# Performance work log

Hardware: AMD Instinct MI355X
Metric: run time of the kernel (lower is better)

The kernel has to match this reference:

```python
import jax, jax.numpy as jnp
import numpy as np

B, T, F = 64, 1000, 512
H, KD = 8, 32
EPS = 1e-6


def setup_inputs() -> dict:
    key = jax.random.key(0)
    ks = jax.random.split(key, 12)
    s_in = 1.0 / np.sqrt(F)
    s_out = 1.0 / np.sqrt(H * KD)
    return {
        "x": jax.random.normal(ks[0], (B, T, F), jnp.float32),
        "q": jax.random.normal(ks[1], (F,), jnp.float32) * s_in,      # global_query (1,1,F) squeezed
        "Wq": jax.random.normal(ks[2], (F, H, KD), jnp.float32) * s_in,
        "bq": jnp.zeros((H, KD), jnp.float32),
        "Wk": jax.random.normal(ks[3], (F, H, KD), jnp.float32) * s_in,
        "bk": jnp.zeros((H, KD), jnp.float32),
        "Wv": jax.random.normal(ks[4], (F, H, KD), jnp.float32) * s_in,
        "bv": jnp.zeros((H, KD), jnp.float32),
        "Wo": jax.random.normal(ks[5], (H, KD, F), jnp.float32) * s_out,
        "bo": jnp.zeros((F,), jnp.float32),
        "Wd": jax.random.normal(ks[6], (F, F), jnp.float32) * s_in,    # Dense, use_bias=False
        "gamma": jnp.ones((F,), jnp.float32),
        "beta": jnp.zeros((F,), jnp.float32),
    }


def reference(x, q, Wq, bq, Wk, bk, Wv, bv, Wo, bo, Wd, gamma, beta):
    # Single learned query attends over full sequence (keras MultiHeadAttention semantics).
    qh = jnp.einsum('f,fhk->hk', q, Wq) + bq                   # (H, KD), shared across batch
    kh = jnp.einsum('btf,fhk->bthk', x, Wk) + bk               # (B, T, H, KD)
    vh = jnp.einsum('btf,fhk->bthk', x, Wv) + bv               # (B, T, H, KD)
    scale = 1.0 / jnp.sqrt(jnp.asarray(KD, x.dtype))
    scores = jnp.einsum('hk,bthk->bht', qh, kh) * scale        # (B, H, T)
    attn = jax.nn.softmax(scores, axis=-1)
    ctx = jnp.einsum('bht,bthk->bhk', attn, vh)                # (B, H, KD)
    pooled = jnp.einsum('bhk,hkf->bf', ctx, Wo) + bo           # (B, F) attention output proj
    out = pooled @ Wd                                          # Dense, no bias
    mu = jnp.mean(out, axis=-1, keepdims=True)
    var = jnp.mean(jnp.square(out - mu), axis=-1, keepdims=True)
    return (out - mu) * jax.lax.rsqrt(var + EPS) * gamma + beta
```

## Files before the change

kernel.cpp:

```cpp
#include <hip/hip_runtime.h>
#include <cstddef>

#define B_ 64
#define T_ 1000
#define F_ 512
#define H_ 8
#define KD_ 32
#define HK_ 256
#define NC_ 32

__global__ __launch_bounds__(64) void k_qh(const float* __restrict__ q,
                                           const float* __restrict__ Wq,
                                           const float* __restrict__ bq,
                                           float* __restrict__ qh) {
    int hk = blockIdx.x;
    int lane = threadIdx.x;
    float s = 0.f;
    for (int f = lane; f < F_; f += 64) s += q[f] * Wq[(size_t)f * HK_ + hk];
    #pragma unroll
    for (int off = 32; off; off >>= 1) s += __shfl_down(s, off);
    if (lane == 0) qh[hk] = s + bq[hk];
}

__global__ __launch_bounds__(256) void k_wk(const float* __restrict__ qh,
                                            const float* __restrict__ Wk,
                                            const float* __restrict__ bk,
                                            float* __restrict__ wk,
                                            float* __restrict__ ck) {
    int f = blockIdx.x;
    int tid = threadIdx.x;
    __shared__ float red[256];
    red[tid] = qh[tid] * Wk[(size_t)f * HK_ + tid];
    __syncthreads();
    #pragma unroll
    for (int off = 16; off; off >>= 1) {
        if ((tid & 31) < off) red[tid] += red[tid + off];
        __syncthreads();
    }
    if ((tid & 31) == 0) wk[f * H_ + (tid >> 5)] = red[tid];
    if (f == 0 && tid < H_) {
        float c = 0.f;
        for (int k = 0; k < KD_; k++) c += qh[tid * KD_ + k] * bk[tid * KD_ + k];
        ck[tid] = c;
    }
}

__global__ __launch_bounds__(512) void k_weff(const float* __restrict__ Wo,
                                              const float* __restrict__ Wd,
                                              const float* __restrict__ bo,
                                              float* __restrict__ weff,
                                              float* __restrict__ bwd) {
    int blk = blockIdx.x;
    int f = threadIdx.x;
    if (blk < HK_) {
        const float* wo = Wo + (size_t)blk * F_;
        float s = 0.f;
        for (int g = 0; g < F_; g++) s += wo[g] * Wd[(size_t)g * F_ + f];
        weff[(size_t)blk * F_ + f] = s;
    } else {
        float s = 0.f;
        for (int g = 0; g < F_; g++) s += bo[g] * Wd[(size_t)g * F_ + f];
        bwd[f] = s;
    }
}

__global__ __launch_bounds__(256) void k_fused(const float* __restrict__ x,
                                               const float* __restrict__ wk,
                                               const float* __restrict__ ck,
                                               float* __restrict__ part,
                                               float* __restrict__ ml) {
    int c = blockIdx.x & (NC_ - 1);
    int b = blockIdx.x >> 5;
    int nt = (c < 8) ? 32 : 31;
    int t0 = (c < 8) ? c * 32 : 256 + (c - 8) * 31;
    int tid = threadIdx.x;
    int lane = tid & 63, w = tid >> 6;

    __shared__ float sp[H_][33];

    {
        int f0 = lane * 8;
        float wreg[8][8];
        #pragma unroll
        for (int i = 0; i < 8; i++)
            #pragma unroll
            for (int h = 0; h < H_; h++) wreg[i][h] = wk[(f0 + i) * H_ + h];
        float ckv = ck[lane >> 3];
        const float scale = 0.17677669529663687f;

        for (int tl = w; tl < nt; tl += 4) {
            const float4* xr = (const float4*)(x + ((size_t)(b * T_ + t0 + tl)) * F_ + f0);
            float4 a = xr[0], bb = xr[1];
            float xv[8] = {a.x, a.y, a.z, a.w, bb.x, bb.y, bb.z, bb.w};
            float acc[8];
            #pragma unroll
            for (int h = 0; h < H_; h++) acc[h] = 0.f;
            #pragma unroll
            for (int i = 0; i < 8; i++)
                #pragma unroll
                for (int h = 0; h < H_; h++) acc[h] += xv[i] * wreg[i][h];
            #pragma unroll
            for (int h = 0; h < H_; h++) {
                acc[h] += __shfl_xor(acc[h], 8);
                acc[h] += __shfl_xor(acc[h], 16);
                acc[h] += __shfl_xor(acc[h], 32);
            }
            float v = acc[0];
            #pragma unroll
            for (int h = 1; h < H_; h++) v = ((lane >> 3) == h) ? acc[h] : v;
            v += __shfl_xor(v, 1);
            v += __shfl_xor(v, 2);
            v += __shfl_xor(v, 4);
            if ((lane & 7) == 0) sp[lane >> 3][tl] = (v + ckv) * scale;
        }
    }
    __syncthreads();

    {
        int g = tid >> 5, j = tid & 31;
        float m = -1e30f;
        if (j < nt) m = sp[g][j];
        #pragma unroll
        for (int off = 16; off; off >>= 1) m = fmaxf(m, __shfl_xor(m, off));
        float e0 = 0.f;
        if (j < nt) e0 = __expf(sp[g][j] - m);
        float l = e0;
        __syncthreads();
        if (j < nt) sp[g][j] = e0;
        #pragma unroll
        for (int off = 16; off; off >>= 1) l += __shfl_xor(l, off);
        if (j == 0) {
            float* d = ml + ((size_t)(c * B_ + b) * H_ + g) * 2;
            d[0] = m; d[1] = l;
        }
    }
    __syncthreads();

    {
        float acc[H_][2];
        #pragma unroll
        for (int h = 0; h < H_; h++) { acc[h][0] = 0.f; acc[h][1] = 0.f; }
        const float2* xb = (const float2*)(x + ((size_t)(b * T_ + t0)) * F_) + tid;
        for (int tt = 0; tt < nt; tt++) {
            float2 xv = xb[(size_t)tt * 256];
            #pragma unroll
            for (int h = 0; h < H_; h++) {
                float a = sp[h][tt];
                acc[h][0] += a * xv.x;
                acc[h][1] += a * xv.y;
            }
        }
        float2* dst = (float2*)(part + (size_t)(c * B_ + b) * (H_ * F_));
        #pragma unroll
        for (int h = 0; h < H_; h++)
            dst[h * (F_ / 2) + tid] = make_float2(acc[h][0], acc[h][1]);
    }
}

__global__ __launch_bounds__(256) void k_ctx(const float* __restrict__ part,
                                             const float* __restrict__ Wv,
                                             float* __restrict__ pctx) {
    int b = blockIdx.x & (B_ - 1);
    int p = blockIdx.x >> 6;
    int hk = threadIdx.x;
    int h = hk >> 5;
    const float* p0 = part + ((size_t)((4 * p + 0) * B_ + b) * H_ + h) * F_;
    const float* p1 = part + ((size_t)((4 * p + 1) * B_ + b) * H_ + h) * F_;
    const float* p2 = part + ((size_t)((4 * p + 2) * B_ + b) * H_ + h) * F_;
    const float* p3 = part + ((size_t)((4 * p + 3) * B_ + b) * H_ + h) * F_;
    float a0 = 0.f, a1 = 0.f, a2 = 0.f, a3 = 0.f;
    for (int f = 0; f < F_; f++) {
        float wv = Wv[(size_t)f * HK_ + hk];
        a0 += p0[f] * wv;
        a1 += p1[f] * wv;
        a2 += p2[f] * wv;
        a3 += p3[f] * wv;
    }
    pctx[((size_t)(4 * p + 0) * B_ + b) * HK_ + hk] = a0;
    pctx[((size_t)(4 * p + 1) * B_ + b) * HK_ + hk] = a1;
    pctx[((size_t)(4 * p + 2) * B_ + b) * HK_ + hk] = a2;
    pctx[((size_t)(4 * p + 3) * B_ + b) * HK_ + hk] = a3;
}

__global__ __launch_bounds__(512) void k_tail(const float* __restrict__ pctx,
                                              const float* __restrict__ ml,
                                              const float* __restrict__ bv,
                                              const float* __restrict__ weff,
                                              const float* __restrict__ bwd,
                                              const float* __restrict__ gamma,
                                              const float* __restrict__ beta,
                                              float* __restrict__ out) {
    int b = blockIdx.x;
    int tid = threadIdx.x;
    __shared__ float coefs[NC_][H_];
    __shared__ float ctx_s[HK_];
    __shared__ float red[16];
    __shared__ float stat[2];

    if (tid < H_) {
        int h = tid;
        float M = -1e30f;
        #pragma unroll
        for (int c = 0; c < NC_; c++)
            M = fmaxf(M, ml[((size_t)(c * B_ + b) * H_ + h) * 2]);
        float L = 0.f;
        #pragma unroll
        for (int c = 0; c < NC_; c++) {
            const float* d = ml + ((size_t)(c * B_ + b) * H_ + h) * 2;
            L += __expf(d[0] - M) * d[1];
        }
        float invL = 1.0f / L;
        #pragma unroll
        for (int c = 0; c < NC_; c++) {
            const float* d = ml + ((size_t)(c * B_ + b) * H_ + h) * 2;
            coefs[c][h] = __expf(d[0] - M) * invL;
        }
    }
    __syncthreads();

    if (tid < HK_) {
        int h = tid >> 5;
        float s = 0.f;
        #pragma unroll
        for (int c = 0; c < NC_; c++)
            s += coefs[c][h] * pctx[((size_t)c * B_ + b) * HK_ + tid];
        ctx_s[tid] = s + bv[tid];
    }
    __syncthreads();

    float o = bwd[tid];
    for (int hk = 0; hk < HK_; hk++) o += ctx_s[hk] * weff[(size_t)hk * F_ + tid];

    {
        float v1 = o, v2 = o * o;
        #pragma unroll
        for (int off = 32; off; off >>= 1) {
            v1 += __shfl_down(v1, off);
            v2 += __shfl_down(v2, off);
        }
        int lane = tid & 63, wid = tid >> 6;
        if (lane == 0) { red[wid] = v1; red[8 + wid] = v2; }
        __syncthreads();
        if (tid == 0) {
            float s1 = 0.f, s2 = 0.f;
            #pragma unroll
            for (int w = 0; w < 8; w++) { s1 += red[w]; s2 += red[8 + w]; }
            float mu = s1 * (1.0f / F_);
            float var = s2 * (1.0f / F_) - mu * mu;
            stat[0] = mu;
            stat[1] = rsqrtf(var + 1e-6f);
        }
        __syncthreads();
    }
    float mu = stat[0], rstd = stat[1];
    out[(size_t)b * F_ + tid] = (o - mu) * rstd * gamma[tid] + beta[tid];
}

extern "C" void kernel_launch(void* const* d_in, const int* in_sizes, int n_in,
                              void* d_out, int out_size, void* d_ws, size_t ws_size,
                              hipStream_t stream) {
    const float* x     = (const float*)d_in[0];
    const float* q     = (const float*)d_in[1];
    const float* Wq    = (const float*)d_in[2];
    const float* bq    = (const float*)d_in[3];
    const float* Wk    = (const float*)d_in[4];
    const float* bk    = (const float*)d_in[5];
    const float* Wv    = (const float*)d_in[6];
    const float* bv    = (const float*)d_in[7];
    const float* Wo    = (const float*)d_in[8];
    const float* bo    = (const float*)d_in[9];
    const float* Wd    = (const float*)d_in[10];
    const float* gamma = (const float*)d_in[11];
    const float* beta  = (const float*)d_in[12];
    float* out = (float*)d_out;

    char* ws = (char*)d_ws;
    float* qh   = (float*)(ws + 0);
    float* wk   = (float*)(ws + 4096);
    float* ck   = (float*)(ws + 20480);
    float* ml   = (float*)(ws + 24576);
    float* weff = (float*)(ws + 262144);
    float* bwd  = (float*)(ws + 786432);
    float* pctx = (float*)(ws + 1048576);
    float* part = (float*)(ws + 4194304);

    k_qh<<<HK_, 64, 0, stream>>>(q, Wq, bq, qh);
    k_wk<<<F_, 256, 0, stream>>>(qh, Wk, bk, wk, ck);
    k_weff<<<HK_ + 1, 512, 0, stream>>>(Wo, Wd, bo, weff, bwd);
    k_fused<<<B_ * NC_, 256, 0, stream>>>(x, wk, ck, part, ml);
    k_ctx<<<(NC_ / 4) * B_, 256, 0, stream>>>(part, Wv, pctx);
    k_tail<<<B_, 512, 0, stream>>>(pctx, ml, bv, weff, bwd, gamma, beta, out);
}
```

Before: 317.8 us.

## Fuse online-softmax attention pooling with Wv projection and stage x through LDS

The main kernel now processes 125-row chunks per (batch, chunk) block with an online softmax. x tiles are double-buffered into shared memory via register prefetch, and each x row is read once from HBM for both scores and weighted accumulation. The Wv projection that used to run in a separate k_ctx kernel is folded into the end of this kernel, so the large per-chunk partial buffer is no longer written and re-read. k_weff is split along the reduction dimension with atomicAdd, which needs a memset first, to expose more parallelism. Fewer chunks (8 instead of 32) reduce grid parallelism and add serial work per block, and the atomics make the sum order nondeterministic.

Measured after the change: 385.0 us. 1.21x slower.

```diff
diff --git a/kernel.cpp b/kernel.cpp
--- a/kernel.cpp
+++ b/kernel.cpp
@@ -7,7 +7,11 @@
 #define H_ 8
 #define KD_ 32
 #define HK_ 256
-#define NC_ 32
+#define NC_ 8
+#define ST_ 16
+#define NST_ 8
+
+#define BAR() do { asm volatile("s_waitcnt lgkmcnt(0)" ::: "memory"); __builtin_amdgcn_s_barrier(); } while (0)
 
 __global__ __launch_bounds__(64) void k_qh(const float* __restrict__ q,
                                            const float* __restrict__ Wq,
@@ -50,140 +54,178 @@
                                               const float* __restrict__ bo,
                                               float* __restrict__ weff,
                                               float* __restrict__ bwd) {
-    int blk = blockIdx.x;
+    int sub = blockIdx.x % 257;
+    int gi = blockIdx.x / 257;
     int f = threadIdx.x;
-    if (blk < HK_) {
-        const float* wo = Wo + (size_t)blk * F_;
+    int g0 = gi * 128;
+    if (sub < HK_) {
+        const float* wo = Wo + (size_t)sub * F_ + g0;
         float s = 0.f;
-        for (int g = 0; g < F_; g++) s += wo[g] * Wd[(size_t)g * F_ + f];
-        weff[(size_t)blk * F_ + f] = s;
+        #pragma unroll 8
+        for (int g = 0; g < 128; g++) s += wo[g] * Wd[(size_t)(g0 + g) * F_ + f];
+        atomicAdd(&weff[(size_t)sub * F_ + f], s);
     } else {
         float s = 0.f;
-        for (int g = 0; g < F_; g++) s += bo[g] * Wd[(size_t)g * F_ + f];
-        bwd[f] = s;
-    }
-}
-
-__global__ __launch_bounds__(256) void k_fused(const float* __restrict__ x,
-                                               const float* __restrict__ wk,
-                                               const float* __restrict__ ck,
-                                               float* __restrict__ part,
-                                               float* __restrict__ ml) {
-    int c = blockIdx.x & (NC_ - 1);
-    int b = blockIdx.x >> 5;
-    int nt = (c < 8) ? 32 : 31;
-    int t0 = (c < 8) ? c * 32 : 256 + (c - 8) * 31;
-    int tid = threadIdx.x;
-    int lane = tid & 63, w = tid >> 6;
-
-    __shared__ float sp[H_][33];
+        #pragma unroll 8
+        for (int g = 0; g < 128; g++) s += bo[g0 + g] * Wd[(size_t)(g0 + g) * F_ + f];
+        atomicAdd(&bwd[f], s);
+    }
+}
+
+__global__ __launch_bounds__(256, 2) void k_fused(const float* __restrict__ x,
+                                                  const float* __restrict__ wk,
+                                                  const float* __restrict__ ck,
+                                                  const float* __restrict__ Wv,
+                                                  float* __restrict__ pctx,
+                                                  float2* __restrict__ ml2) {
+    __shared__ __align__(16) float buf[2][ST_ * F_];
+    __shared__ __align__(16) float sp[ST_][H_];
+    __shared__ __align__(16) float facL[H_];
+
+    const int c = blockIdx.x & (NC_ - 1);
+    const int b = blockIdx.x >> 3;
+    const int tid = threadIdx.x;
+    const int lane = tid & 63;
+    const int w = tid >> 6;
+    const int h0i = 2 * w, h1i = 2 * w + 1;
+    const int f0 = lane * 8;
+    const float scale = 0.17677669529663687f;
+
+    float w0[8], w1[8];
+    #pragma unroll
+    for (int i = 0; i < 8; i++) {
+        w0[i] = wk[(f0 + i) * H_ + h0i];
+        w1[i] = wk[(f0 + i) * H_ + h1i];
+    }
+    const float ck0 = ck[h0i], ck1 = ck[h1i];
+
+    float m0 = -3.0e38f, m1 = -3.0e38f, l0 = 0.f, l1 = 0.f;
+    float accx[8], accy[8];
+    #pragma unroll
+    for (int h = 0; h < 8; h++) { accx[h] = 0.f; accy[h] = 0.f; }
+
+    const float* gbase = x + ((size_t)b * T_ + c * 125) * F_;
+    float4 rr[8];
 
     {
-        int f0 = lane * 8;
-        float wreg[8][8];
+        const char* src = (const char*)(gbase);
         #pragma unroll
         for (int i = 0; i < 8; i++)
+            rr[i] = *(const float4*)(src + i * 4096 + tid * 16);
+        char* dst = (char*)&buf[0][0];
+        #pragma unroll
+        for (int i = 0; i < 8; i++)
+            *(float4*)(dst + i * 4096 + tid * 16) = rr[i];
+        const char* src1 = (const char*)(gbase + (size_t)ST_ * F_);
+        #pragma unroll
+        for (int i = 0; i < 8; i++)
+            rr[i] = *(const float4*)(src1 + i * 4096 + tid * 16);
+        BAR();
+    }
+
+    for (int st = 0; st < NST_; st++) {
+        const int cur = st & 1;
+        const float* bc = &buf[cur][0];
+        const int nval = 125 - st * ST_;
+
+        float s0[ST_], s1[ST_];
+        #pragma unroll
+        for (int r = 0; r < ST_; r++) {
+            if (r < nval) {
+                const float4 a0 = *(const float4*)&bc[r * F_ + f0];
+                const float4 a1 = *(const float4*)&bc[r * F_ + f0 + 4];
+                float v0 = a0.x*w0[0] + a0.y*w0[1] + a0.z*w0[2] + a0.w*w0[3]
+                         + a1.x*w0[4] + a1.y*w0[5] + a1.z*w0[6] + a1.w*w0[7];
+                float v1 = a0.x*w1[0] + a0.y*w1[1] + a0.z*w1[2] + a0.w*w1[3]
+                         + a1.x*w1[4] + a1.y*w1[5] + a1.z*w1[6] + a1.w*w1[7];
+                #pragma unroll
+                for (int msk = 1; msk < 64; msk <<= 1) {
+                    v0 += __shfl_xor(v0, msk);
+                    v1 += __shfl_xor(v1, msk);
+                }
+                s0[r] = (v0 + ck0) * scale;
+                s1[r] = (v1 + ck1) * scale;
+            } else {
+                s0[r] = -3.0e38f; s1[r] = -3.0e38f;
+            }
+        }
+        float mt0 = s0[0], mt1 = s1[0];
+        #pragma unroll
+        for (int r = 1; r < ST_; r++) { mt0 = fmaxf(mt0, s0[r]); mt1 = fmaxf(mt1, s1[r]); }
+        const float mn0 = fmaxf(m0, mt0), mn1 = fmaxf(m1, mt1);
+        const float fc0 = __expf(m0 - mn0), fc1 = __expf(m1 - mn1);
+        float lt0 = 0.f, lt1 = 0.f;
+        #pragma unroll
+        for (int r = 0; r < ST_; r++) {
+            const float p0 = __expf(s0[r] - mn0);
+            const float p1 = __expf(s1[r] - mn1);
+            lt0 += p0; lt1 += p1;
+            if (lane == 0) { sp[r][h0i] = p0; sp[r][h1i] = p1; }
+        }
+        l0 = l0 * fc0 + lt0;  m0 = mn0;
+        l1 = l1 * fc1 + lt1;  m1 = mn1;
+        if (lane == 0) { facL[h0i] = fc0; facL[h1i] = fc1; }
+
+        BAR();
+
+        {
+            const float4 fA = *(const float4*)&facL[0];
+            const float4 fB = *(const float4*)&facL[4];
+            const float fv[8] = {fA.x, fA.y, fA.z, fA.w, fB.x, fB.y, fB.z, fB.w};
             #pragma unroll
-            for (int h = 0; h < H_; h++) wreg[i][h] = wk[(f0 + i) * H_ + h];
-        float ckv = ck[lane >> 3];
-        const float scale = 0.17677669529663687f;
-
-        for (int tl = w; tl < nt; tl += 4) {
-            const float4* xr = (const float4*)(x + ((size_t)(b * T_ + t0 + tl)) * F_ + f0);
-            float4 a = xr[0], bb = xr[1];
-            float xv[8] = {a.x, a.y, a.z, a.w, bb.x, bb.y, bb.z, bb.w};
-            float acc[8];
+            for (int h = 0; h < 8; h++) { accx[h] *= fv[h]; accy[h] *= fv[h]; }
             #pragma unroll
-            for (int h = 0; h < H_; h++) acc[h] = 0.f;
+            for (int r = 0; r < ST_; r++) {
+                const float2 xv = *(const float2*)&bc[r * F_ + 2 * tid];
+                const float4 pa = *(const float4*)&sp[r][0];
+                const float4 pb = *(const float4*)&sp[r][4];
+                const float pv[8] = {pa.x, pa.y, pa.z, pa.w, pb.x, pb.y, pb.z, pb.w};
+                #pragma unroll
+                for (int h = 0; h < 8; h++) { accx[h] += pv[h] * xv.x; accy[h] += pv[h] * xv.y; }
+            }
+        }
+
+        if (st < NST_ - 1) {
+            char* dst = (char*)&buf[cur ^ 1][0];
             #pragma unroll
             for (int i = 0; i < 8; i++)
+                *(float4*)(dst + i * 4096 + tid * 16) = rr[i];
+            if (st < NST_ - 2) {
+                const int ts = st + 2;
+                const int nv = 125 - ts * ST_;
+                const int vb = (nv > 16 ? 16 : nv) * 2048;
+                const char* src = (const char*)(gbase + (size_t)ts * ST_ * F_);
                 #pragma unroll
-                for (int h = 0; h < H_; h++) acc[h] += xv[i] * wreg[i][h];
-            #pragma unroll
-            for (int h = 0; h < H_; h++) {
-                acc[h] += __shfl_xor(acc[h], 8);
-                acc[h] += __shfl_xor(acc[h], 16);
-                acc[h] += __shfl_xor(acc[h], 32);
+                for (int i = 0; i < 8; i++) {
+                    const int off = i * 4096 + tid * 16;
+                    if (off < vb) rr[i] = *(const float4*)(src + off);
+                }
             }
-            float v = acc[0];
-            #pragma unroll
-            for (int h = 1; h < H_; h++) v = ((lane >> 3) == h) ? acc[h] : v;
-            v += __shfl_xor(v, 1);
-            v += __shfl_xor(v, 2);
-            v += __shfl_xor(v, 4);
-            if ((lane & 7) == 0) sp[lane >> 3][tl] = (v + ckv) * scale;
-        }
-    }
-    __syncthreads();
-
+        }
+        BAR();
+    }
+
+    float* accL = &buf[0][0];
+    #pragma unroll
+    for (int h = 0; h < 8; h++)
+        *(float2*)&accL[h * F_ + 2 * tid] = make_float2(accx[h], accy[h]);
+    BAR();
     {
-        int g = tid >> 5, j = tid & 31;
-        float m = -1e30f;
-        if (j < nt) m = sp[g][j];
-        #pragma unroll
-        for (int off = 16; off; off >>= 1) m = fmaxf(m, __shfl_xor(m, off));
-        float e0 = 0.f;
-        if (j < nt) e0 = __expf(sp[g][j] - m);
-        float l = e0;
-        __syncthreads();
-        if (j < nt) sp[g][j] = e0;
-        #pragma unroll
-        for (int off = 16; off; off >>= 1) l += __shfl_xor(l, off);
-        if (j == 0) {
-            float* d = ml + ((size_t)(c * B_ + b) * H_ + g) * 2;
-            d[0] = m; d[1] = l;
-        }
-    }
-    __syncthreads();
-
-    {
-        float acc[H_][2];
-        #pragma unroll
-        for (int h = 0; h < H_; h++) { acc[h][0] = 0.f; acc[h][1] = 0.f; }
-        const float2* xb = (const float2*)(x + ((size_t)(b * T_ + t0)) * F_) + tid;
-        for (int tt = 0; tt < nt; tt++) {
-            float2 xv = xb[(size_t)tt * 256];
-            #pragma unroll
-            for (int h = 0; h < H_; h++) {
-                float a = sp[h][tt];
-                acc[h][0] += a * xv.x;
-                acc[h][1] += a * xv.y;
-            }
-        }
-        float2* dst = (float2*)(part + (size_t)(c * B_ + b) * (H_ * F_));
-        #pragma unroll
-        for (int h = 0; h < H_; h++)
-            dst[h * (F_ / 2) + tid] = make_float2(acc[h][0], acc[h][1]);
-    }
-}
-
-__global__ __launch_bounds__(256) void k_ctx(const float* __restrict__ part,
-                                             const float* __restrict__ Wv,
-                                             float* __restrict__ pctx) {
-    int b = blockIdx.x & (B_ - 1);
-    int p = blockIdx.x >> 6;
-    int hk = threadIdx.x;
-    int h = hk >> 5;
-    const float* p0 = part + ((size_t)((4 * p + 0) * B_ + b) * H_ + h) * F_;
-    const float* p1 = part + ((size_t)((4 * p + 1) * B_ + b) * H_ + h) * F_;
-    const float* p2 = part + ((size_t)((4 * p + 2) * B_ + b) * H_ + h) * F_;
-    const float* p3 = part + ((size_t)((4 * p + 3) * B_ + b) * H_ + h) * F_;
-    float a0 = 0.f, a1 = 0.f, a2 = 0.f, a3 = 0.f;
-    for (int f = 0; f < F_; f++) {
-        float wv = Wv[(size_t)f * HK_ + hk];
-        a0 += p0[f] * wv;
-        a1 += p1[f] * wv;
-        a2 += p2[f] * wv;
-        a3 += p3[f] * wv;
-    }
-    pctx[((size_t)(4 * p + 0) * B_ + b) * HK_ + hk] = a0;
-    pctx[((size_t)(4 * p + 1) * B_ + b) * HK_ + hk] = a1;
-    pctx[((size_t)(4 * p + 2) * B_ + b) * HK_ + hk] = a2;
-    pctx[((size_t)(4 * p + 3) * B_ + b) * HK_ + hk] = a3;
+        const int h = tid >> 5;
+        const float* aL = &accL[h * F_];
+        float s = 0.f;
+        #pragma unroll 8
+        for (int f = 0; f < F_; f++) s += aL[f] * Wv[(size_t)f * HK_ + tid];
+        pctx[((size_t)b * NC_ + c) * HK_ + tid] = s;
+    }
+    if (lane == 0) {
+        ml2[((size_t)b * NC_ + c) * H_ + h0i] = make_float2(m0, l0);
+        ml2[((size_t)b * NC_ + c) * H_ + h1i] = make_float2(m1, l1);
+    }
 }
 
 __global__ __launch_bounds__(512) void k_tail(const float* __restrict__ pctx,
-                                              const float* __restrict__ ml,
+                                              const float2* __restrict__ ml2,
                                               const float* __restrict__ bv,
                                               const float* __restrict__ weff,
                                               const float* __restrict__ bwd,
@@ -192,28 +234,28 @@
                                               float* __restrict__ out) {
     int b = blockIdx.x;
     int tid = threadIdx.x;
-    __shared__ float coefs[NC_][H_];
+    __shared__ float coef[NC_][H_];
     __shared__ float ctx_s[HK_];
     __shared__ float red[16];
     __shared__ float stat[2];
 
     if (tid < H_) {
         int h = tid;
-        float M = -1e30f;
+        float M = -3.0e38f;
         #pragma unroll
         for (int c = 0; c < NC_; c++)
-            M = fmaxf(M, ml[((size_t)(c * B_ + b) * H_ + h) * 2]);
+            M = fmaxf(M, ml2[((size_t)b * NC_ + c) * H_ + h].x);
         float L = 0.f;
         #pragma unroll
         for (int c = 0; c < NC_; c++) {
-            const float* d = ml + ((size_t)(c * B_ + b) * H_ + h) * 2;
-            L += __expf(d[0] - M) * d[1];
+            float2 d = ml2[((size_t)b * NC_ + c) * H_ + h];
+            L += __expf(d.x - M) * d.y;
         }
         float invL = 1.0f / L;
         #pragma unroll
         for (int c = 0; c < NC_; c++) {
-            const float* d = ml + ((size_t)(c * B_ + b) * H_ + h) * 2;
-            coefs[c][h] = __expf(d[0] - M) * invL;
+            float2 d = ml2[((size_t)b * NC_ + c) * H_ + h];
+            coef[c][h] = __expf(d.x - M) * invL;
         }
     }
     __syncthreads();
@@ -223,12 +265,13 @@
         float s = 0.f;
         #pragma unroll
         for (int c = 0; c < NC_; c++)
-            s += coefs[c][h] * pctx[((size_t)c * B_ + b) * HK_ + tid];
+            s += coef[c][h] * pctx[((size_t)b * NC_ + c) * HK_ + tid];
         ctx_s[tid] = s + bv[tid];
     }
     __syncthreads();
 
     float o = bwd[tid];
+    #pragma unroll 8
     for (int hk = 0; hk < HK_; hk++) o += ctx_s[hk] * weff[(size_t)hk * F_ + tid];
 
     {
@@ -244,7 +287,7 @@
         if (tid == 0) {
             float s1 = 0.f, s2 = 0.f;
             #pragma unroll
-            for (int w = 0; w < 8; w++) { s1 += red[w]; s2 += red[8 + w]; }
+            for (int ww = 0; ww < 8; ww++) { s1 += red[ww]; s2 += red[8 + ww]; }
             float mu = s1 * (1.0f / F_);
             float var = s2 * (1.0f / F_) - mu * mu;
             stat[0] = mu;
@@ -275,19 +318,18 @@
     float* out = (float*)d_out;
 
     char* ws = (char*)d_ws;
-    float* qh   = (float*)(ws + 0);
-    float* wk   = (float*)(ws + 4096);
-    float* ck   = (float*)(ws + 20480);
-    float* ml   = (float*)(ws + 24576);
-    float* weff = (float*)(ws + 262144);
-    float* bwd  = (float*)(ws + 786432);
-    float* pctx = (float*)(ws + 1048576);
-    float* part = (float*)(ws + 4194304);
-
+    float*  qh   = (float*)(ws + 0);
+    float*  wk   = (float*)(ws + 4096);
+    float*  ck   = (float*)(ws + 20480);
+    float*  weff = (float*)(ws + 24576);
+    float*  bwd  = (float*)(ws + 548864);
+    float2* ml2  = (float2*)(ws + 557056);
+    float*  pctx = (float*)(ws + 589824);
+
+    hipMemsetAsync(ws + 24576, 0, 526336, stream);
     k_qh<<<HK_, 64, 0, stream>>>(q, Wq, bq, qh);
     k_wk<<<F_, 256, 0, stream>>>(qh, Wk, bk, wk, ck);
-    k_weff<<<HK_ + 1, 512, 0, stream>>>(Wo, Wd, bo, weff, bwd);
-    k_fused<<<B_ * NC_, 256, 0, stream>>>(x, wk, ck, part, ml);
-    k_ctx<<<(NC_ / 4) * B_, 256, 0, stream>>>(part, Wv, pctx);
-    k_tail<<<B_, 512, 0, stream>>>(pctx, ml, bv, weff, bwd, gamma, beta, out);
-}
+    k_weff<<<4 * 257, 512, 0, stream>>>(Wo, Wd, bo, weff, bwd);
+    k_fused<<<B_ * NC_, 256, 0, stream>>>(x, wk, ck, Wv, pctx, ml2);
+    k_tail<<<B_, 512, 0, stream>>>(pctx, ml2, bv, weff, bwd, gamma, beta, out);
+}
```
